# Optimization experiments

Measured on AMD Instinct MI355X. Metric: run time of the kernel, lower is better.

## Reference

```python
import jax, jax.numpy as jnp
import numpy as np

LAMDA = 0.5
BATCH_SIZE = 1024
MARGIN = 0.5
NEG_OFFSET = 100000.0
INTRA_MARGIN = 0.1
EPS = 1e-12


def setup_inputs() -> dict:
    key = jax.random.key(0)
    k1, k2, k3 = jax.random.split(key, 3)
    feat = jax.random.normal(k1, (2 * BATCH_SIZE, 128), dtype=jnp.float32)
    label1 = jax.random.randint(k2, (BATCH_SIZE,), 0, 128, dtype=jnp.int64)
    label2 = jax.random.randint(k3, (BATCH_SIZE,), 0, 128, dtype=jnp.int64)
    return {"feat": feat, "label1": label1, "label2": label2}


def _cdist(a, b):
    # faithful to source: broadcasted diff, sqrt(sum(d^2) + 1e-12)
    diffs = a[:, None, :] - b[None, :, :]          # [N, M, D]
    return jnp.sqrt(jnp.sum(diffs * diffs, axis=-1) + EPS)


def _half(f_a, f_b, lab_a, lab_b, f_intra, margin):
    dis = _cdist(f_a, f_b)                          # [B, B]
    s = (lab_a[:, None] == lab_b[None, :]).astype(dis.dtype)
    furthest_positive = jnp.max(dis * s, axis=1)
    pos_positive = jnp.argmax(dis * s, axis=1)
    closest_negative = jnp.min(dis + NEG_OFFSET * s, axis=1)
    pos_negative = jnp.argmin(dis + NEG_OFFSET * s, axis=1)
    cross = jnp.mean(jnp.clip(furthest_positive - closest_negative + margin, 0.0))
    dis_intra = _cdist(f_intra, f_intra)            # [B, B]
    gathered = dis_intra[pos_positive, pos_negative]  # gather_2d equivalent
    intra = jnp.mean(jnp.clip(INTRA_MARGIN - gathered, 0.0))
    return cross, intra


def reference(feat, label1, label2):
    feature1 = feat[:BATCH_SIZE]
    feature2 = feat[BATCH_SIZE:]
    cross1, intra1 = _half(feature1, feature2, label1, label2, feature2, MARGIN)
    cross2, intra2 = _half(feature2, feature1, label2, label1, feature1, MARGIN)
    return (cross1 + cross2) + LAMDA * (intra1 + intra2)
```

## Files before the change

### kernel.cpp

```cpp
#include <hip/hip_runtime.h>
#include <math.h>
#include <float.h>

#define BATCH 1024
#define DIM 128
#define EPSV 1e-12f
#define MARGIN 0.5f
#define INTRA_MARGIN 0.1f
#define LAMDA 0.5f

typedef __attribute__((ext_vector_type(8))) short s16x8;
typedef __attribute__((ext_vector_type(4))) float f32x4;

__device__ __forceinline__ ushort f2bf(float f) {
    unsigned u = __float_as_uint(f);
    return (ushort)((u + 0x7fffu + ((u >> 16) & 1u)) >> 16);
}

__device__ __forceinline__ void gl_lds16(const void* g, void* l) {
    __builtin_amdgcn_global_load_lds(
        (const __attribute__((address_space(1))) unsigned int*)g,
        (__attribute__((address_space(3))) unsigned int*)l,
        16, 0, 0);
}

#define WAITVM8()  do { asm volatile("s_waitcnt vmcnt(8)" ::: "memory"); __builtin_amdgcn_sched_barrier(0); } while (0)
#define WAITVM4()  do { asm volatile("s_waitcnt vmcnt(4)" ::: "memory"); __builtin_amdgcn_sched_barrier(0); } while (0)
#define WAITVM0()  do { asm volatile("s_waitcnt vmcnt(0)" ::: "memory"); __builtin_amdgcn_sched_barrier(0); } while (0)

__global__ __launch_bounds__(256) void prep_kernel(
    const float* __restrict__ feat, ushort* __restrict__ bhi,
    float* __restrict__ norm2)
{
    const int t = threadIdx.x;
    const int gt  = blockIdx.x * 256 + t;
    const int row = gt >> 4, seg = gt & 15;
    const float4* p = reinterpret_cast<const float4*>(feat + (size_t)row * DIM + seg * 8);
    const float4 a = p[0], b = p[1];
    const float v[8] = {a.x, a.y, a.z, a.w, b.x, b.y, b.z, b.w};
    ushort h[8];
    float n = 0.0f;
    #pragma unroll
    for (int e = 0; e < 8; ++e) {
        h[e] = f2bf(v[e]);
        n = fmaf(v[e], v[e], n);
    }
    uint4 uh;
    uh.x = (uint)h[0] | ((uint)h[1] << 16); uh.y = (uint)h[2] | ((uint)h[3] << 16);
    uh.z = (uint)h[4] | ((uint)h[5] << 16); uh.w = (uint)h[6] | ((uint)h[7] << 16);
    reinterpret_cast<uint4*>(bhi)[row * 16 + (seg ^ (row & 7))] = uh;
    n += __shfl_xor(n, 1); n += __shfl_xor(n, 2);
    n += __shfl_xor(n, 4); n += __shfl_xor(n, 8);
    if ((t & 15) == 0) norm2[row] = n;
}

__device__ __forceinline__ void issue_chunk(const char* bbytes, size_t gbase,
                                            char* buf, int w, int lane) {
    #pragma unroll
    for (int i = 0; i < 4; ++i) {
        const int o = w * 4096 + i * 1024 + lane * 16;
        gl_lds16(bbytes + gbase + o, buf + o);
    }
}

__global__ __launch_bounds__(512, 1) void gemm_kernel(
    const ushort* __restrict__ bhi, const float* __restrict__ norm2,
    const float* __restrict__ feat,
    const int* __restrict__ label1, const int* __restrict__ label2,
    float* __restrict__ partial)
{
    __shared__ __align__(16) char smem[131072];

    const int rg    = blockIdx.x;
    const int half  = rg >> 7;
    const int arow0 = (rg & 127) * 8;
    const int aglob0 = half * BATCH + arow0;
    const int bglob0 = (half ^ 1) * BATCH;

    const int t = threadIdx.x;
    const int w = t >> 6, lane = t & 63;
    const int l15 = lane & 15, kg = lane >> 4;

    const int* labA = half ? label2 : label1;
    const int* labB = half ? label1 : label2;

    float nb[8]; int lb[8];
    #pragma unroll
    for (int c = 0; c < 8; ++c) {
        const int jc = c * 128 + w * 16 + l15;
        nb[c] = norm2[bglob0 + jc];
        lb[c] = labB[jc];
    }
    float na[4]; int la[4];
    #pragma unroll
    for (int r = 0; r < 4; ++r) {
        const int rr = (kg * 4 + r) & 7;
        na[r] = norm2[aglob0 + rr];
        la[r] = labA[arow0 + rr];
    }

    s16x8 ah[4];
    const size_t abase = (size_t)(aglob0 + (l15 & 7)) * DIM;
    #pragma unroll
    for (int kt = 0; kt < 4; ++kt) {
        const int kh = (kt * 32 + kg * 8) ^ ((l15 & 7) << 3);
        ah[kt] = *reinterpret_cast<const s16x8*>(bhi + abase + kh);
    }

    const char* bbytes = reinterpret_cast<const char*>(bhi);
    issue_chunk(bbytes, (size_t)(bglob0 + 0 * 128) * 256, smem + 0 * 32768, w, lane);
    issue_chunk(bbytes, (size_t)(bglob0 + 1 * 128) * 256, smem + 1 * 32768, w, lane);
    issue_chunk(bbytes, (size_t)(bglob0 + 2 * 128) * 256, smem + 2 * 32768, w, lane);
    WAITVM8();

    float bpv[4], bnv[4]; int bpj[4], bnj[4];
    #pragma unroll
    for (int r = 0; r < 4; ++r) { bpv[r] = -1.0f; bpj[r] = 0x7fffffff; bnv[r] = FLT_MAX; bnj[r] = 0x7fffffff; }

    const int jl = w * 16 + l15;

    #pragma unroll
    for (int c = 0; c < 8; ++c) {
        const ushort* bufc = reinterpret_cast<const ushort*>(smem + (c & 3) * 32768);

        s16x8 bh[4];
        #pragma unroll
        for (int kt = 0; kt < 4; ++kt) {
            const int kh = (kt * 32 + kg * 8) ^ ((l15 & 7) << 3);
            bh[kt] = *reinterpret_cast<const s16x8*>(bufc + jl * DIM + kh);
        }
        if (c <= 4)
            issue_chunk(bbytes, (size_t)(bglob0 + (c + 3) * 128) * 256,
                        smem + ((c + 3) & 3) * 32768, w, lane);

        f32x4 acc = (f32x4){0.f, 0.f, 0.f, 0.f};
        #pragma unroll
        for (int kt = 0; kt < 4; ++kt)
            acc = __builtin_amdgcn_mfma_f32_16x16x32_bf16(ah[kt], bh[kt], acc, 0, 0, 0);

        const int jc = c * 128 + jl;
        #pragma unroll
        for (int r = 0; r < 4; ++r) {
            const float d2 = fmaxf(na[r] + nb[c] - 2.0f * acc[r], 0.0f);
            const bool same = (la[r] == lb[c]);
            const float pv = same ? d2 : 0.0f;
            const float nv = same ? FLT_MAX : d2;
            if (pv > bpv[r]) { bpv[r] = pv; bpj[r] = jc; }
            if (nv < bnv[r]) { bnv[r] = nv; bnj[r] = jc; }
        }

        if (c <= 4)      WAITVM8();
        else if (c == 5) WAITVM4();
        else if (c == 6) WAITVM0();
    }

    #pragma unroll
    for (int r = 0; r < 4; ++r) {
        #pragma unroll
        for (int m = 8; m > 0; m >>= 1) {
            const float opv = __shfl_xor(bpv[r], m); const int opj = __shfl_xor(bpj[r], m);
            if (opv > bpv[r] || (opv == bpv[r] && opj < bpj[r])) { bpv[r] = opv; bpj[r] = opj; }
            const float onv = __shfl_xor(bnv[r], m); const int onj = __shfl_xor(bnj[r], m);
            if (onv < bnv[r] || (onv == bnv[r] && onj < bnj[r])) { bnv[r] = onv; bnj[r] = onj; }
        }
    }

    __syncthreads();

    float (*L_pv)[8] = (float(*)[8])(smem);
    int   (*L_pj)[8] = (int  (*)[8])(smem + 512);
    float (*L_nv)[8] = (float(*)[8])(smem + 1024);
    int   (*L_nj)[8] = (int  (*)[8])(smem + 1536);
    int*   s_pp = (int*)  (smem + 2048);
    int*   s_pn = (int*)  (smem + 2112);
    float* s_fp = (float*)(smem + 2176);
    float* s_cn = (float*)(smem + 2240);
    float* ls   = (float*)(smem + 2304);

    if (l15 == 0) {
        #pragma unroll
        for (int r = 0; r < 4; ++r) {
            const int rib = kg * 4 + r;
            L_pv[rib][w] = bpv[r]; L_pj[rib][w] = bpj[r];
            L_nv[rib][w] = bnv[r]; L_nj[rib][w] = bnj[r];
        }
    }
    __syncthreads();

    if (t < 8) {
        float pv = -1.0f; int pj = 0x7fffffff; float nv = FLT_MAX; int nj = 0x7fffffff;
        #pragma unroll
        for (int c = 0; c < 8; ++c) {
            const float v1 = L_pv[t][c]; const int j1 = L_pj[t][c];
            if (v1 > pv || (v1 == pv && j1 < pj)) { pv = v1; pj = j1; }
            const float v2 = L_nv[t][c]; const int j2 = L_nj[t][c];
            if (v2 < nv || (v2 == nv && j2 < nj)) { nv = v2; nj = j2; }
        }
        s_pp[t] = pj > (BATCH - 1) ? (BATCH - 1) : pj;
        s_pn[t] = nj > (BATCH - 1) ? (BATCH - 1) : nj;
        s_fp[t] = (pv > 0.0f) ? sqrtf(pv + EPSV) : 0.0f;
        s_cn[t] = sqrtf(nv + EPSV);
    }
    __syncthreads();

    if (t < 128) {
        const int g = t >> 4, sl = t & 15;
        const float* fB = feat + (size_t)(half ^ 1) * BATCH * DIM;
        const float4* x = reinterpret_cast<const float4*>(fB + (size_t)s_pp[g] * DIM + sl * 8);
        const float4* y = reinterpret_cast<const float4*>(fB + (size_t)s_pn[g] * DIM + sl * 8);
        const float4 x0 = x[0], x1 = x[1], y0 = y[0], y1 = y[1];
        float d, d2;
        d = x0.x - y0.x; d2  = d * d;  d = x0.y - y0.y; d2 += d * d;
        d = x0.z - y0.z; d2 += d * d;  d = x0.w - y0.w; d2 += d * d;
        d = x1.x - y1.x; d2 += d * d;  d = x1.y - y1.y; d2 += d * d;
        d = x1.z - y1.z; d2 += d * d;  d = x1.w - y1.w; d2 += d * d;
        d2 += __shfl_xor(d2, 1); d2 += __shfl_xor(d2, 2);
        d2 += __shfl_xor(d2, 4); d2 += __shfl_xor(d2, 8);
        if (sl == 0) {
            const float gd = sqrtf(d2 + EPSV);
            const float loss = fmaxf(s_fp[g] - s_cn[g] + MARGIN, 0.0f)
                             + LAMDA * fmaxf(INTRA_MARGIN - gd, 0.0f);
            ls[g] = loss * (1.0f / (float)BATCH);
        }
    }
    __syncthreads();

    if (t == 0) {
        float s = 0.0f;
        #pragma unroll
        for (int i = 0; i < 8; ++i) s += ls[i];
        partial[rg] = s;
    }
}

__global__ __launch_bounds__(64) void reduce_kernel(
    const float* __restrict__ partial, float* __restrict__ out)
{
    const int t = threadIdx.x;
    float s = partial[t] + partial[t + 64] + partial[t + 128] + partial[t + 192];
    #pragma unroll
    for (int m = 32; m > 0; m >>= 1) s += __shfl_down(s, m);
    if (t == 0) out[0] = s;
}

extern "C" void kernel_launch(void* const* d_in, const int* in_sizes, int n_in,
                              void* d_out, int out_size, void* d_ws, size_t ws_size,
                              hipStream_t stream) {
    const float* feat   = (const float*)d_in[0];
    const int*   label1 = (const int*)d_in[1];
    const int*   label2 = (const int*)d_in[2];
    float* out = (float*)d_out;

    char* ws = (char*)d_ws;
    float*  partial = (float*)(ws);
    ushort* bhi     = (ushort*)(ws + 4096);
    float*  norm2   = (float*)(ws + 4096 + 512 * 1024);

    prep_kernel<<<dim3(128), dim3(256), 0, stream>>>(feat, bhi, norm2);
    gemm_kernel<<<dim3(256), dim3(512), 0, stream>>>(
        bhi, norm2, feat, label1, label2, partial);
    reduce_kernel<<<dim3(1), dim3(64), 0, stream>>>(partial, out);
}
```

Before: 20.91 us.

## Fuse bf16 conversion and norm computation into the distance GEMM kernel

Removes the separate prep kernel that converted features to bf16 and computed squared norms. The main kernel now streams fp32 B-tiles into LDS with a swizzled layout, converts to bf16 in registers, and computes row norms on the fly with shuffles, using double buffering instead of a quad buffer. This saves one kernel launch and the intermediate workspace round trip. In exchange each block loads twice the bytes per chunk, runs a shallower prefetch pipeline, and redoes the conversion work across 128 blocks per half.

```diff
diff --git a/kernel.cpp b/kernel.cpp
--- a/kernel.cpp
+++ b/kernel.cpp
@@ -17,6 +17,19 @@
     return (ushort)((u + 0x7fffu + ((u >> 16) & 1u)) >> 16);
 }
 
+__device__ __forceinline__ s16x8 cvt8(float4 a, float4 b, float& ss) {
+    s16x8 r;
+    r[0] = (short)f2bf(a.x); ss = fmaf(a.x, a.x, ss);
+    r[1] = (short)f2bf(a.y); ss = fmaf(a.y, a.y, ss);
+    r[2] = (short)f2bf(a.z); ss = fmaf(a.z, a.z, ss);
+    r[3] = (short)f2bf(a.w); ss = fmaf(a.w, a.w, ss);
+    r[4] = (short)f2bf(b.x); ss = fmaf(b.x, b.x, ss);
+    r[5] = (short)f2bf(b.y); ss = fmaf(b.y, b.y, ss);
+    r[6] = (short)f2bf(b.z); ss = fmaf(b.z, b.z, ss);
+    r[7] = (short)f2bf(b.w); ss = fmaf(b.w, b.w, ss);
+    return r;
+}
+
 __device__ __forceinline__ void gl_lds16(const void* g, void* l) {
     __builtin_amdgcn_global_load_lds(
         (const __attribute__((address_space(1))) unsigned int*)g,
@@ -25,46 +38,23 @@
 }
 
 #define WAITVM8()  do { asm volatile("s_waitcnt vmcnt(8)" ::: "memory"); __builtin_amdgcn_sched_barrier(0); } while (0)
-#define WAITVM4()  do { asm volatile("s_waitcnt vmcnt(4)" ::: "memory"); __builtin_amdgcn_sched_barrier(0); } while (0)
 #define WAITVM0()  do { asm volatile("s_waitcnt vmcnt(0)" ::: "memory"); __builtin_amdgcn_sched_barrier(0); } while (0)
-
-__global__ __launch_bounds__(256) void prep_kernel(
-    const float* __restrict__ feat, ushort* __restrict__ bhi,
-    float* __restrict__ norm2)
-{
-    const int t = threadIdx.x;
-    const int gt  = blockIdx.x * 256 + t;
-    const int row = gt >> 4, seg = gt & 15;
-    const float4* p = reinterpret_cast<const float4*>(feat + (size_t)row * DIM + seg * 8);
-    const float4 a = p[0], b = p[1];
-    const float v[8] = {a.x, a.y, a.z, a.w, b.x, b.y, b.z, b.w};
-    ushort h[8];
-    float n = 0.0f;
-    #pragma unroll
-    for (int e = 0; e < 8; ++e) {
-        h[e] = f2bf(v[e]);
-        n = fmaf(v[e], v[e], n);
-    }
-    uint4 uh;
-    uh.x = (uint)h[0] | ((uint)h[1] << 16); uh.y = (uint)h[2] | ((uint)h[3] << 16);
-    uh.z = (uint)h[4] | ((uint)h[5] << 16); uh.w = (uint)h[6] | ((uint)h[7] << 16);
-    reinterpret_cast<uint4*>(bhi)[row * 16 + (seg ^ (row & 7))] = uh;
-    n += __shfl_xor(n, 1); n += __shfl_xor(n, 2);
-    n += __shfl_xor(n, 4); n += __shfl_xor(n, 8);
-    if ((t & 15) == 0) norm2[row] = n;
-}
-
-__device__ __forceinline__ void issue_chunk(const char* bbytes, size_t gbase,
-                                            char* buf, int w, int lane) {
-    #pragma unroll
-    for (int i = 0; i < 4; ++i) {
-        const int o = w * 4096 + i * 1024 + lane * 16;
-        gl_lds16(bbytes + gbase + o, buf + o);
-    }
-}
-
-__global__ __launch_bounds__(512, 1) void gemm_kernel(
-    const ushort* __restrict__ bhi, const float* __restrict__ norm2,
+#define WAITLGKM() do { asm volatile("s_waitcnt lgkmcnt(0)" ::: "memory"); __builtin_amdgcn_sched_barrier(0); } while (0)
+
+__device__ __forceinline__ void issue_chunk_f32(const char* fbytes, int grow0,
+                                                char* buf, int w, int lane) {
+    #pragma unroll
+    for (int i = 0; i < 8; ++i) {
+        const int s   = i * 64 + lane;
+        const int rho = s >> 5;
+        const int u   = (lane & 31) ^ (rho & 7);
+        const size_t src = (size_t)(grow0 + w * 16 + rho) * 512 + (size_t)u * 16;
+        const int dst = w * 8192 + i * 1024 + lane * 16;
+        gl_lds16(fbytes + src, buf + dst);
+    }
+}
+
+__global__ __launch_bounds__(512, 1) void fused_kernel(
     const float* __restrict__ feat,
     const int* __restrict__ label1, const int* __restrict__ label2,
     float* __restrict__ partial)
@@ -84,54 +74,63 @@
     const int* labA = half ? label2 : label1;
     const int* labB = half ? label1 : label2;
 
-    float nb[8]; int lb[8];
+    int lb[8];
+    #pragma unroll
+    for (int c = 0; c < 8; ++c) lb[c] = labB[c * 128 + w * 16 + l15];
+    int la[4];
+    #pragma unroll
+    for (int r = 0; r < 4; ++r) la[r] = labA[arow0 + ((kg * 4 + r) & 7)];
+
+    const float* arow = feat + (size_t)(aglob0 + (l15 & 7)) * DIM;
+    s16x8 ah[4];
+    float naL = 0.0f;
+    #pragma unroll
+    for (int kt = 0; kt < 4; ++kt) {
+        const float4 a0 = *reinterpret_cast<const float4*>(arow + kt * 32 + kg * 8);
+        const float4 a1 = *reinterpret_cast<const float4*>(arow + kt * 32 + kg * 8 + 4);
+        ah[kt] = cvt8(a0, a1, naL);
+    }
+    naL += __shfl_xor(naL, 16); naL += __shfl_xor(naL, 32);
+    float na[4];
+    #pragma unroll
+    for (int r = 0; r < 4; ++r) na[r] = __shfl(naL, kg * 4 + r);
+
+    const char* fbytes = reinterpret_cast<const char*>(feat);
+    __builtin_amdgcn_sched_barrier(0);
+    issue_chunk_f32(fbytes, bglob0 + 0 * 128, smem,         w, lane);
+    issue_chunk_f32(fbytes, bglob0 + 1 * 128, smem + 65536, w, lane);
+    WAITVM8();
+
+    float bpv[4], bnv[4]; int bpj[4], bnj[4];
+    #pragma unroll
+    for (int r = 0; r < 4; ++r) { bpv[r] = -1.0f; bpj[r] = 0x7fffffff; bnv[r] = FLT_MAX; bnj[r] = 0x7fffffff; }
+
+    const int jl = w * 16 + l15;
+
     #pragma unroll
     for (int c = 0; c < 8; ++c) {
-        const int jc = c * 128 + w * 16 + l15;
-        nb[c] = norm2[bglob0 + jc];
-        lb[c] = labB[jc];
-    }
-    float na[4]; int la[4];
-    #pragma unroll
-    for (int r = 0; r < 4; ++r) {
-        const int rr = (kg * 4 + r) & 7;
-        na[r] = norm2[aglob0 + rr];
-        la[r] = labA[arow0 + rr];
-    }
-
-    s16x8 ah[4];
-    const size_t abase = (size_t)(aglob0 + (l15 & 7)) * DIM;
-    #pragma unroll
-    for (int kt = 0; kt < 4; ++kt) {
-        const int kh = (kt * 32 + kg * 8) ^ ((l15 & 7) << 3);
-        ah[kt] = *reinterpret_cast<const s16x8*>(bhi + abase + kh);
-    }
-
-    const char* bbytes = reinterpret_cast<const char*>(bhi);
-    issue_chunk(bbytes, (size_t)(bglob0 + 0 * 128) * 256, smem + 0 * 32768, w, lane);
-    issue_chunk(bbytes, (size_t)(bglob0 + 1 * 128) * 256, smem + 1 * 32768, w, lane);
-    issue_chunk(bbytes, (size_t)(bglob0 + 2 * 128) * 256, smem + 2 * 32768, w, lane);
-    WAITVM8();
-
-    float bpv[4], bnv[4]; int bpj[4], bnj[4];
-    #pragma unroll
-    for (int r = 0; r < 4; ++r) { bpv[r] = -1.0f; bpj[r] = 0x7fffffff; bnv[r] = FLT_MAX; bnj[r] = 0x7fffffff; }
-
-    const int jl = w * 16 + l15;
-
-    #pragma unroll
-    for (int c = 0; c < 8; ++c) {
-        const ushort* bufc = reinterpret_cast<const ushort*>(smem + (c & 3) * 32768);
-
+        const char* bufc = smem + (c & 1) * 65536;
+
+        float4 bv[8];
+        #pragma unroll
+        for (int kt = 0; kt < 4; ++kt) {
+            const int u0 = kt * 8 + kg * 2;
+            bv[2 * kt]     = *reinterpret_cast<const float4*>(
+                bufc + w * 8192 + l15 * 512 + ((u0    ) ^ (l15 & 7)) * 16);
+            bv[2 * kt + 1] = *reinterpret_cast<const float4*>(
+                bufc + w * 8192 + l15 * 512 + ((u0 + 1) ^ (l15 & 7)) * 16);
+        }
+        WAITLGKM();
+        if (c <= 5)
+            issue_chunk_f32(fbytes, bglob0 + (c + 2) * 128,
+                            smem + (c & 1) * 65536, w, lane);
+
+        float nbL = 0.0f;
         s16x8 bh[4];
         #pragma unroll
-        for (int kt = 0; kt < 4; ++kt) {
-            const int kh = (kt * 32 + kg * 8) ^ ((l15 & 7) << 3);
-            bh[kt] = *reinterpret_cast<const s16x8*>(bufc + jl * DIM + kh);
-        }
-        if (c <= 4)
-            issue_chunk(bbytes, (size_t)(bglob0 + (c + 3) * 128) * 256,
-                        smem + ((c + 3) & 3) * 32768, w, lane);
+        for (int kt = 0; kt < 4; ++kt)
+            bh[kt] = cvt8(bv[2 * kt], bv[2 * kt + 1], nbL);
+        nbL += __shfl_xor(nbL, 16); nbL += __shfl_xor(nbL, 32);
 
         f32x4 acc = (f32x4){0.f, 0.f, 0.f, 0.f};
         #pragma unroll
@@ -141,7 +140,7 @@
         const int jc = c * 128 + jl;
         #pragma unroll
         for (int r = 0; r < 4; ++r) {
-            const float d2 = fmaxf(na[r] + nb[c] - 2.0f * acc[r], 0.0f);
+            const float d2 = fmaxf(na[r] + nbL - 2.0f * acc[r], 0.0f);
             const bool same = (la[r] == lb[c]);
             const float pv = same ? d2 : 0.0f;
             const float nv = same ? FLT_MAX : d2;
@@ -149,8 +148,7 @@
             if (nv < bnv[r]) { bnv[r] = nv; bnj[r] = jc; }
         }
 
-        if (c <= 4)      WAITVM8();
-        else if (c == 5) WAITVM4();
+        if (c <= 5)      WAITVM8();
         else if (c == 6) WAITVM0();
     }
 
@@ -251,13 +249,8 @@
     const int*   label2 = (const int*)d_in[2];
     float* out = (float*)d_out;
 
-    char* ws = (char*)d_ws;
-    float*  partial = (float*)(ws);
-    ushort* bhi     = (ushort*)(ws + 4096);
-    float*  norm2   = (float*)(ws + 4096 + 512 * 1024);
-
-    prep_kernel<<<dim3(128), dim3(256), 0, stream>>>(feat, bhi, norm2);
-    gemm_kernel<<<dim3(256), dim3(512), 0, stream>>>(
-        bhi, norm2, feat, label1, label2, partial);
+    float* partial = (float*)d_ws;
+
+    fused_kernel<<<dim3(256), dim3(512), 0, stream>>>(feat, label1, label2, partial);
     reduce_kernel<<<dim3(1), dim3(64), 0, stream>>>(partial, out);
 }
```

Result: slower. 22.97 us (+9.8%).
